# Performance work log

Hardware: AMD Instinct MI355X
Metric: run time of the kernel (lower is better)

Reference implementation:

```python
import jax, jax.numpy as jnp
import numpy as np

DN = ('NCHW', 'OIHW', 'NCHW')

def conv(x, w, b=None, pad=0):
    y = jax.lax.conv_general_dilated(x, w, (1, 1), [(pad, pad), (pad, pad)], dimension_numbers=DN)
    if b is not None:
        y = y + b[None, :, None, None]
    return y

def bn(x, g, b):
    # inference-mode BatchNorm with running_mean=0, running_var=1 (affine only)
    return g[None, :, None, None] * x + b[None, :, None, None]

def gru(msg, h, wg, bg, wc, g, be):
    gates = conv(jnp.concatenate([msg, h], axis=1), wg, bg)  # [B,2,H,W]
    r = jax.nn.sigmoid(gates[:, 0:1])
    u = jax.nn.sigmoid(gates[:, 1:2])
    cnm = jax.nn.leaky_relu(bn(conv(jnp.concatenate([msg, r * h], axis=1), wc), g, be), 0.01)
    return (1.0 - u) * h + u * cnm

def setup_inputs() -> dict:
    key = jax.random.key(0)
    ks = jax.random.split(key, 32)
    B, C, H, W = 8, 10, 192, 192
    s = 0.1
    inp = {
        'f_nodes': jax.random.normal(ks[0], (2, B, C, H, W), jnp.float32),
        'h_nodes': jax.random.normal(ks[1], (3, B, C, H, W), jnp.float32),
        'p_nodes': jax.random.normal(ks[2], (7, B, C, H, W), jnp.float32),
        'xh': jax.random.normal(ks[3], (B, C, H, W), jnp.float32),
        # Decomp_att: 1x1 conv 30->3
        'w_dmap': jax.random.normal(ks[4], (3, 30, 1, 1)) * s,
        'b_dmap': jnp.zeros((3,)),
        # Decomposition relation (shared across 2 children): 3x3 conv 20->10 + BN
        'w_decomp': jax.random.normal(ks[5], (10, 20, 3, 3)) * s,
        'g_decomp': jnp.ones((10,)), 'be_decomp': jnp.zeros((10,)),
        # Comp_att upper: 1x1 conv 40->1 ; lower: 20->1
        'w_cau': jax.random.normal(ks[6], (1, 40, 1, 1)) * s, 'b_cau': jnp.zeros((1,)),
        'w_cal': jax.random.normal(ks[7], (1, 20, 1, 1)) * s, 'b_cal': jnp.zeros((1,)),
        # Composition relation (shared across parts): 3x3 conv 20->10 + BN
        'w_cu': jax.random.normal(ks[8], (10, 20, 3, 3)) * s,
        'g_cu': jnp.ones((10,)), 'be_cu': jnp.zeros((10,)),
        'w_cl': jax.random.normal(ks[9], (10, 20, 3, 3)) * s,
        'g_cl': jnp.ones((10,)), 'be_cl': jnp.zeros((10,)),
        # ConvGRU upper: gates 1x1 20->2, candidate 1x1 20->10 + ABN(leaky_relu)
        'wg_u': jax.random.normal(ks[10], (2, 20, 1, 1)) * s, 'bg_u': jnp.zeros((2,)),
        'wc_u': jax.random.normal(ks[11], (10, 20, 1, 1)) * s,
        'g_u': jnp.ones((10,)), 'be_u': jnp.zeros((10,)),
        # ConvGRU lower
        'wg_l': jax.random.normal(ks[12], (2, 20, 1, 1)) * s, 'bg_l': jnp.zeros((2,)),
        'wc_l': jax.random.normal(ks[13], (10, 20, 1, 1)) * s,
        'g_l': jnp.ones((10,)), 'be_l': jnp.zeros((10,)),
    }
    return inp

def reference(f_nodes, h_nodes, p_nodes, xh,
              w_dmap, b_dmap, w_decomp, g_decomp, be_decomp,
              w_cau, b_cau, w_cal, b_cal,
              w_cu, g_cu, be_cu, w_cl, g_cl, be_cl,
              wg_u, bg_u, wc_u, g_u, be_u,
              wg_l, bg_l, wc_l, g_l, be_l):
    f1 = f_nodes[1]
    h1, h2 = h_nodes[1], h_nodes[2]

    # Decomp_att: 1x1 conv over [f1, h1, h2]
    decomp_map = conv(jnp.concatenate([f1, h1, h2], axis=1), w_dmap, b_dmap)  # [B,3,H,W]
    att = jax.nn.softmax(decomp_map, axis=1)

    # Decomposition (channels 0 is parent-self slot; children use slots 1,2)
    d0 = jax.nn.relu(bn(conv(jnp.concatenate([f1 * att[:, 1:2], h1], axis=1), w_decomp, pad=1), g_decomp, be_decomp))
    d1 = jax.nn.relu(bn(conv(jnp.concatenate([f1 * att[:, 2:3], h2], axis=1), w_decomp, pad=1), g_decomp, be_decomp))

    # Upper half: parts 1..4
    upper = [p_nodes[i] for i in (1, 2, 3, 4)]
    comp_map_u = jax.nn.sigmoid(conv(jnp.concatenate(upper, axis=1), w_cau, b_cau))  # [B,1,H,W]
    comp_u = sum(jax.nn.relu(bn(conv(jnp.concatenate([h1, c * comp_map_u], axis=1), w_cu, pad=1), g_cu, be_cu)) for c in upper)
    msg_u = d0 + comp_u
    xh_u = gru(msg_u, h1, wg_u, bg_u, wc_u, g_u, be_u)

    # Lower half: parts 5..6
    lower = [p_nodes[i] for i in (5, 6)]
    comp_map_l = jax.nn.sigmoid(conv(jnp.concatenate(lower, axis=1), w_cal, b_cal))
    comp_l = sum(jax.nn.relu(bn(conv(jnp.concatenate([h2, c * comp_map_l], axis=1), w_cl, pad=1), g_cl, be_cl)) for c in lower)
    msg_l = d1 + comp_l
    xh_l = gru(msg_l, h2, wg_l, bg_l, wc_l, g_l, be_l)

    xh_new = jnp.stack([h_nodes[0], xh_u, xh_l], axis=0)  # [3,B,10,H,W]
    return (xh_new, decomp_map, comp_map_u, comp_map_l)
```

## Files before the change

kernel.cpp:

```cpp
#include <hip/hip_runtime.h>

#define HW 36864
#define WD 192
#define BB 8
#define CC 10
#define PW 194
#define PB ((size_t)(PW*PW*16))
#define PA ((size_t)BB*PB)

typedef __attribute__((ext_vector_type(8))) short short8;
typedef __attribute__((ext_vector_type(4))) float f32x4;

__device__ __forceinline__ short f2bf(float v) {
    unsigned u = __float_as_uint(v);
    unsigned r = (u + 0x7fffu + ((u >> 16) & 1u)) >> 16;
    return (short)r;
}
__device__ __forceinline__ float b2f(short s) {
    return __uint_as_float(((unsigned)(unsigned short)s) << 16);
}

#define ASYNC16(gp, lp) __builtin_amdgcn_global_load_lds( \
    (const __attribute__((address_space(1))) void*)(gp),  \
    (__attribute__((address_space(3))) void*)(lp), 16, 0, 0)

__device__ __forceinline__ void store16(short* d, const float* v, float s) {
    short8 lo, hi;
    #pragma unroll
    for (int i = 0; i < 8; ++i) lo[i] = f2bf(v[i]*s);
    hi = (short8){f2bf(v[8]*s), f2bf(v[9]*s), 0,0,0,0,0,0};
    *(short8*)d = lo;
    *(short8*)(d+8) = hi;
}

__global__ __launch_bounds__(256) void prep_kernel(
    const float* __restrict__ f_nodes, const float* __restrict__ h_nodes,
    const float* __restrict__ p_nodes,
    const float* __restrict__ w_dmap, const float* __restrict__ b_dmap,
    const float* __restrict__ w_cau, const float* __restrict__ b_cau,
    const float* __restrict__ w_cal, const float* __restrict__ b_cal,
    float* __restrict__ out, short* __restrict__ ws)
{
    int t = blockIdx.x*256 + threadIdx.x;
    if (t >= BB*PW*PW) return;
    int b  = t / (PW*PW);
    int pp = t - b*(PW*PW);
    int py = pp / PW, px = pp - py*PW;
    short* wb = ws + (size_t)b*PB + (size_t)pp*16;

    if (py == 0 || py == PW-1 || px == 0 || px == PW-1) {
        short8 z = (short8){0,0,0,0,0,0,0,0};
        #pragma unroll
        for (int a = 0; a < 10; ++a) {
            *(short8*)(wb + (size_t)a*PA)     = z;
            *(short8*)(wb + (size_t)a*PA + 8) = z;
        }
        return;
    }
    int sp = (py-1)*WD + (px-1);

    const float* f1 = f_nodes + ((size_t)(BB   + b))*CC*HW + sp;
    const float* h0 = h_nodes + ((size_t)(       b))*CC*HW + sp;
    const float* h1 = h_nodes + ((size_t)(BB   + b))*CC*HW + sp;
    const float* h2 = h_nodes + ((size_t)(2*BB + b))*CC*HW + sp;

    float fv[10], av[10], bv[10];
    #pragma unroll
    for (int c = 0; c < 10; ++c) {
        fv[c] = f1[(size_t)c*HW];
        av[c] = h1[(size_t)c*HW];
        bv[c] = h2[(size_t)c*HW];
    }

    const size_t O1 = (size_t)3*BB*CC*HW;
    const size_t O2 = O1 + (size_t)BB*3*HW;
    const size_t O3 = O2 + (size_t)BB*HW;

    float dm[3];
    #pragma unroll
    for (int j = 0; j < 3; ++j) {
        float s = b_dmap[j];
        #pragma unroll
        for (int c = 0; c < 10; ++c) s = fmaf(w_dmap[j*30 + c],      fv[c], s);
        #pragma unroll
        for (int c = 0; c < 10; ++c) s = fmaf(w_dmap[j*30 + 10 + c], av[c], s);
        #pragma unroll
        for (int c = 0; c < 10; ++c) s = fmaf(w_dmap[j*30 + 20 + c], bv[c], s);
        dm[j] = s;
        out[O1 + ((size_t)b*3 + j)*HW + sp] = s;
    }
    float mx = fmaxf(dm[0], fmaxf(dm[1], dm[2]));
    float e0 = expf(dm[0]-mx), e1 = expf(dm[1]-mx), e2 = expf(dm[2]-mx);
    float inv = 1.f / (e0 + e1 + e2);
    float a1 = e1*inv, a2 = e2*inv;

    store16(wb + 0*PA, av, 1.f);
    store16(wb + 1*PA, bv, 1.f);
    store16(wb + 2*PA, fv, a1);
    store16(wb + 3*PA, fv, a2);

    float* o0 = out + (size_t)b*CC*HW + sp;
    #pragma unroll
    for (int c = 0; c < 10; ++c) o0[(size_t)c*HW] = h0[(size_t)c*HW];

    {
        float pv[4][10];
        float su = b_cau[0];
        #pragma unroll
        for (int i = 0; i < 4; ++i) {
            const float* p = p_nodes + ((size_t)((1+i)*BB + b))*CC*HW + sp;
            #pragma unroll
            for (int c = 0; c < 10; ++c) pv[i][c] = p[(size_t)c*HW];
            #pragma unroll
            for (int c = 0; c < 10; ++c) su = fmaf(w_cau[i*10 + c], pv[i][c], su);
        }
        float cmU = 1.f / (1.f + expf(-su));
        out[O2 + (size_t)b*HW + sp] = cmU;
        #pragma unroll
        for (int i = 0; i < 4; ++i) store16(wb + (size_t)(4+i)*PA, pv[i], cmU);
    }
    {
        float qv[2][10];
        float sl = b_cal[0];
        #pragma unroll
        for (int i = 0; i < 2; ++i) {
            const float* p = p_nodes + ((size_t)((5+i)*BB + b))*CC*HW + sp;
            #pragma unroll
            for (int c = 0; c < 10; ++c) qv[i][c] = p[(size_t)c*HW];
            #pragma unroll
            for (int c = 0; c < 10; ++c) sl = fmaf(w_cal[i*10 + c], qv[i][c], sl);
        }
        float cmL = 1.f / (1.f + expf(-sl));
        out[O3 + (size_t)b*HW + sp] = cmL;
        #pragma unroll
        for (int i = 0; i < 2; ++i) store16(wb + (size_t)(8+i)*PA, qv[i], cmL);
    }
}

__device__ __forceinline__ void dma_tile(short* lds, const short* g,
                                         int tid, int y0, int x0)
{
    #pragma unroll
    for (int r = 0; r < 3; ++r) {
        int idx = r*256 + tid;
        int row = idx / 36;
        int col = idx - row*36;
        size_t go = (idx < 648) ? (((size_t)(y0+row)*PW + x0)*16 + (size_t)col*8)
                                : (size_t)0;
        ASYNC16(g + go, lds + (size_t)idx*8);
    }
}

__global__ __launch_bounds__(256) void half_kernel(
    const short* __restrict__ ws,
    const float* __restrict__ w_dec, const float* __restrict__ gD, const float* __restrict__ bD,
    const float* __restrict__ w_cu, const float* __restrict__ gCu, const float* __restrict__ bCu,
    const float* __restrict__ w_cl, const float* __restrict__ gCl, const float* __restrict__ bCl,
    const float* __restrict__ wg_u, const float* __restrict__ bg_u, const float* __restrict__ wc_u,
    const float* __restrict__ g_u, const float* __restrict__ be_u,
    const float* __restrict__ wg_l, const float* __restrict__ bg_l, const float* __restrict__ wc_l,
    const float* __restrict__ g_l, const float* __restrict__ be_l,
    float* __restrict__ out)
{
    __shared__ __align__(16) short sTh[6144];
    __shared__ __align__(16) short sTp0[6144];
    __shared__ __align__(16) short sTp1[6144];
    __shared__ __align__(16) short sWb[4*2688];
    __shared__ float sMsg[256*13];
    __shared__ float sPar[302];

    const int tid  = threadIdx.x;
    const int lane = tid & 63;
    const int w    = tid >> 6;
    const int g    = lane >> 4;
    const int n    = lane & 15;
    const int half = blockIdx.z >> 3;
    const int b    = blockIdx.z & 7;
    const int x0   = blockIdx.x*16, y0 = blockIdx.y*16;

    const float* w_cmp = half ? w_cl : w_cu;
    const float* gC  = half ? gCl  : gCu;
    const float* bC  = half ? bCl  : bCu;
    const float* wg  = half ? wg_l : wg_u;
    const float* bg  = half ? bg_l : bg_u;
    const float* wc  = half ? wc_l : wc_u;
    const float* gG  = half ? g_l  : g_u;
    const float* beG = half ? be_l : be_u;
    const int nparts = half ? 2 : 4;

    const short* hArr  = ws + (size_t)half*PA     + (size_t)b*PB;
    const short* fArr  = ws + (size_t)(2+half)*PA + (size_t)b*PB;
    const short* pArr0 = ws + (size_t)(4+half*4)*PA + (size_t)b*PB;

    for (int i = tid; i < 4*2688/2; i += 256) ((int*)sWb)[i] = 0;
    dma_tile(sTh,  hArr,  tid, y0, x0);
    dma_tile(sTp0, fArr,  tid, y0, x0);
    dma_tile(sTp1, pArr0, tid, y0, x0);
    __syncthreads();

    for (int i = tid; i < 1800; i += 256) {
        int o = i/180, r = i - o*180, ci = r/9, kp = r - ci*9;
        int c  = (ci < 10) ? ci : ci - 10;
        int s2 = (ci < 10) ? 0 : 1;
        sWb[s2*2688     + o*168 + kp*16 + c] = f2bf(w_dec[i]);
        sWb[(2+s2)*2688 + o*168 + kp*16 + c] = f2bf(w_cmp[i]);
    }
    if (tid < 10) {
        sPar[tid]    = gD[tid];  sPar[10+tid] = bD[tid];
        sPar[20+tid] = gC[tid];  sPar[30+tid] = bC[tid];
        sPar[40+tid] = gG[tid];  sPar[50+tid] = beG[tid];
    }
    if (tid < 40) sPar[60+tid]  = wg[tid];
    if (tid < 2)  sPar[100+tid] = bg[tid];
    if (tid >= 56 && tid < 256) sPar[102+(tid-56)] = (tid-56 < 200) ? wc[tid-56] : 0.f;
    __syncthreads();

    int aoff[5];
    #pragma unroll
    for (int t5 = 0; t5 < 5; ++t5) {
        int k  = 32*t5 + 8*g;
        int kp = k >> 4;
        int c8 = k & 15;
        if (kp < 9) { int ky = kp/3, kx = kp - ky*3; aoff[t5] = (ky*18 + kx + n)*16 + c8; }
        else        aoff[t5] = 0;
    }
    const int wbase = w*4*288;

    short8 bF[5], bH[5], bCh[5], bCp[5];
    #pragma unroll
    for (int t5 = 0; t5 < 5; ++t5) {
        int ko = 32*t5 + 8*g;
        bF[t5]  = *(const short8*)(sWb + 0*2688 + n*168 + ko);
        bH[t5]  = *(const short8*)(sWb + 1*2688 + n*168 + ko);
        bCh[t5] = *(const short8*)(sWb + 2*2688 + n*168 + ko);
        bCp[t5] = *(const short8*)(sWb + 3*2688 + n*168 + ko);
    }

    f32x4 accD[4], accH[4];
    #pragma unroll
    for (int mt = 0; mt < 4; ++mt) { accD[mt] = (f32x4){0,0,0,0}; accH[mt] = (f32x4){0,0,0,0}; }
    #pragma unroll
    for (int t5 = 0; t5 < 5; ++t5) {
        #pragma unroll
        for (int mt = 0; mt < 4; ++mt) {
            short8 a = *(const short8*)(sTp0 + wbase + mt*288 + aoff[t5]);
            accD[mt] = __builtin_amdgcn_mfma_f32_16x16x32_bf16(a, bF[t5], accD[mt], 0,0,0);
        }
    }
    #pragma unroll
    for (int t5 = 0; t5 < 5; ++t5) {
        #pragma unroll
        for (int mt = 0; mt < 4; ++mt) {
            short8 a = *(const short8*)(sTh + wbase + mt*288 + aoff[t5]);
            accD[mt] = __builtin_amdgcn_mfma_f32_16x16x32_bf16(a, bH[t5],  accD[mt], 0,0,0);
            accH[mt] = __builtin_amdgcn_mfma_f32_16x16x32_bf16(a, bCh[t5], accH[mt], 0,0,0);
        }
    }
    const int np = (n < 10) ? n : 9;
    const float gDv = sPar[np],    bDv = sPar[10+np];
    const float gCv = sPar[20+np], bCv = sPar[30+np];
    f32x4 msgf[4];
    #pragma unroll
    for (int mt = 0; mt < 4; ++mt)
        #pragma unroll
        for (int j = 0; j < 4; ++j)
            msgf[mt][j] = fmaxf(fmaf(gDv, accD[mt][j], bDv), 0.f);
    __syncthreads();

    for (int j = 0; j < nparts; ++j) {
        if (j+1 < nparts)
            dma_tile((j&1) ? sTp1 : sTp0, pArr0 + (size_t)(j+1)*PA, tid, y0, x0);
        const short* cur = (j&1) ? sTp0 : sTp1;
        f32x4 acc[4];
        #pragma unroll
        for (int mt = 0; mt < 4; ++mt) acc[mt] = (f32x4){0,0,0,0};
        #pragma unroll
        for (int t5 = 0; t5 < 5; ++t5) {
            #pragma unroll
            for (int mt = 0; mt < 4; ++mt) {
                short8 a = *(const short8*)(cur + wbase + mt*288 + aoff[t5]);
                acc[mt] = __builtin_amdgcn_mfma_f32_16x16x32_bf16(a, bCp[t5], acc[mt], 0,0,0);
            }
        }
        #pragma unroll
        for (int mt = 0; mt < 4; ++mt)
            #pragma unroll
            for (int jj = 0; jj < 4; ++jj)
                msgf[mt][jj] += fmaxf(fmaf(gCv, accH[mt][jj] + acc[mt][jj], bCv), 0.f);
        __syncthreads();
    }

    if (n < 10) {
        #pragma unroll
        for (int mt = 0; mt < 4; ++mt)
            #pragma unroll
            for (int r2 = 0; r2 < 4; ++r2)
                sMsg[((4*w + mt)*16 + 4*g + r2)*13 + n] = msgf[mt][r2];
    }
    __syncthreads();

    {
        int row = tid >> 4, xx = tid & 15;
        int gy = y0 + row, gx = x0 + xx;
        float msg[10], hc[10];
        #pragma unroll
        for (int c = 0; c < 10; ++c) msg[c] = sMsg[tid*13 + c];
        #pragma unroll
        for (int c = 0; c < 10; ++c) hc[c] = b2f(sTh[((row+1)*18 + (xx+1))*16 + c]);

        float g0 = sPar[100], g1 = sPar[101];
        #pragma unroll
        for (int c = 0; c < 10; ++c) {
            g0 = fmaf(sPar[60+c], msg[c], g0);
            g1 = fmaf(sPar[80+c], msg[c], g1);
        }
        #pragma unroll
        for (int c = 0; c < 10; ++c) {
            g0 = fmaf(sPar[70+c], hc[c], g0);
            g1 = fmaf(sPar[90+c], hc[c], g1);
        }
        float r = 1.f / (1.f + expf(-g0));
        float u = 1.f / (1.f + expf(-g1));

        float* op = out + (size_t)(1+half)*BB*CC*HW + (size_t)b*CC*HW + gy*WD + gx;
        #pragma unroll
        for (int o = 0; o < 10; ++o) {
            float s = 0.f;
            const float* wr = &sPar[102 + o*20];
            #pragma unroll
            for (int c = 0; c < 10; ++c) s = fmaf(wr[c], msg[c], s);
            #pragma unroll
            for (int c = 0; c < 10; ++c) s = fmaf(wr[10+c], r*hc[c], s);
            s = fmaf(sPar[40+o], s, sPar[50+o]);
            s = (s > 0.f) ? s : 0.01f*s;
            op[(size_t)o*HW] = (1.f - u)*hc[o] + u*s;
        }
    }
}

extern "C" void kernel_launch(void* const* d_in, const int* in_sizes, int n_in,
                              void* d_out, int out_size, void* d_ws, size_t ws_size,
                              hipStream_t stream)
{
    const float* f_nodes = (const float*)d_in[0];
    const float* h_nodes = (const float*)d_in[1];
    const float* p_nodes = (const float*)d_in[2];
    const float* w_dmap   = (const float*)d_in[4];
    const float* b_dmap   = (const float*)d_in[5];
    const float* w_decomp = (const float*)d_in[6];
    const float* g_decomp = (const float*)d_in[7];
    const float* be_decomp= (const float*)d_in[8];
    const float* w_cau    = (const float*)d_in[9];
    const float* b_cau    = (const float*)d_in[10];
    const float* w_cal    = (const float*)d_in[11];
    const float* b_cal    = (const float*)d_in[12];
    const float* w_cu     = (const float*)d_in[13];
    const float* g_cu     = (const float*)d_in[14];
    const float* be_cu    = (const float*)d_in[15];
    const float* w_cl     = (const float*)d_in[16];
    const float* g_cl     = (const float*)d_in[17];
    const float* be_cl    = (const float*)d_in[18];
    const float* wg_u     = (const float*)d_in[19];
    const float* bg_u     = (const float*)d_in[20];
    const float* wc_u     = (const float*)d_in[21];
    const float* g_u      = (const float*)d_in[22];
    const float* be_u     = (const float*)d_in[23];
    const float* wg_l     = (const float*)d_in[24];
    const float* bg_l     = (const float*)d_in[25];
    const float* wc_l     = (const float*)d_in[26];
    const float* g_l      = (const float*)d_in[27];
    const float* be_l     = (const float*)d_in[28];

    float* out = (float*)d_out;
    short* ws  = (short*)d_ws;

    prep_kernel<<<dim3((BB*PW*PW + 255)/256), dim3(256), 0, stream>>>(
        f_nodes, h_nodes, p_nodes, w_dmap, b_dmap,
        w_cau, b_cau, w_cal, b_cal, out, ws);

    half_kernel<<<dim3(WD/16, WD/16, 16), dim3(256), 0, stream>>>(
        ws, w_decomp, g_decomp, be_decomp,
        w_cu, g_cu, be_cu, w_cl, g_cl, be_cl,
        wg_u, bg_u, wc_u, g_u, be_u,
        wg_l, bg_l, wc_l, g_l, be_l,
        out);
}
```

Before: 317.3 us.

## Vectorize prep into float4 work groups and precompute bf16 weights once

The prep kernel now gives each thread four adjacent pixels using float4 loads and stores. Work is split across three block groups (decomposition, upper parts, lower parts), and border zeroing and weight packing go to extra blocks. The conv weights and per-half parameters are converted to bf16 and packed into the workspace once, so half_kernel no longer rebuilds them in LDS in every block. half_kernel reads its B operands straight from global or cache, which removes an LDS buffer and a barrier, at the cost of global reads in the MFMA setup.

```diff
diff --git a/kernel.cpp b/kernel.cpp
--- a/kernel.cpp
+++ b/kernel.cpp
@@ -7,9 +7,13 @@
 #define PW 194
 #define PB ((size_t)(PW*PW*16))
 #define PA ((size_t)BB*PB)
+#define WSW_OFF ((size_t)10*PA)
+#define NWSW 15360
 
 typedef __attribute__((ext_vector_type(8))) short short8;
 typedef __attribute__((ext_vector_type(4))) float f32x4;
+
+__device__ __forceinline__ f32x4 sp4(float x) { return (f32x4){x, x, x, x}; }
 
 __device__ __forceinline__ short f2bf(float v) {
     unsigned u = __float_as_uint(v);
@@ -24,13 +28,17 @@
     (const __attribute__((address_space(1))) void*)(gp),  \
     (__attribute__((address_space(3))) void*)(lp), 16, 0, 0)
 
-__device__ __forceinline__ void store16(short* d, const float* v, float s) {
-    short8 lo, hi;
-    #pragma unroll
-    for (int i = 0; i < 8; ++i) lo[i] = f2bf(v[i]*s);
-    hi = (short8){f2bf(v[8]*s), f2bf(v[9]*s), 0,0,0,0,0,0};
-    *(short8*)d = lo;
-    *(short8*)(d+8) = hi;
+__device__ __forceinline__ void store4(short* d, const f32x4* v, f32x4 s) {
+    #pragma unroll
+    for (int i = 0; i < 4; ++i) {
+        short8 lo = { f2bf(v[0][i]*s[i]), f2bf(v[1][i]*s[i]),
+                      f2bf(v[2][i]*s[i]), f2bf(v[3][i]*s[i]),
+                      f2bf(v[4][i]*s[i]), f2bf(v[5][i]*s[i]),
+                      f2bf(v[6][i]*s[i]), f2bf(v[7][i]*s[i]) };
+        short8 hi = { f2bf(v[8][i]*s[i]), f2bf(v[9][i]*s[i]), 0,0,0,0,0,0 };
+        *(short8*)(d + i*16)     = lo;
+        *(short8*)(d + i*16 + 8) = hi;
+    }
 }
 
 __global__ __launch_bounds__(256) void prep_kernel(
@@ -39,101 +47,172 @@
     const float* __restrict__ w_dmap, const float* __restrict__ b_dmap,
     const float* __restrict__ w_cau, const float* __restrict__ b_cau,
     const float* __restrict__ w_cal, const float* __restrict__ b_cal,
+    const float* __restrict__ w_decomp, const float* __restrict__ w_cu,
+    const float* __restrict__ w_cl,
+    const float* __restrict__ g_decomp, const float* __restrict__ be_decomp,
+    const float* __restrict__ g_cu, const float* __restrict__ be_cu,
+    const float* __restrict__ g_cl, const float* __restrict__ be_cl,
+    const float* __restrict__ wg_u, const float* __restrict__ bg_u,
+    const float* __restrict__ wc_u, const float* __restrict__ g_u,
+    const float* __restrict__ be_u,
+    const float* __restrict__ wg_l, const float* __restrict__ bg_l,
+    const float* __restrict__ wc_l, const float* __restrict__ g_l,
+    const float* __restrict__ be_l,
     float* __restrict__ out, short* __restrict__ ws)
 {
-    int t = blockIdx.x*256 + threadIdx.x;
-    if (t >= BB*PW*PW) return;
-    int b  = t / (PW*PW);
-    int pp = t - b*(PW*PW);
-    int py = pp / PW, px = pp - py*PW;
-    short* wb = ws + (size_t)b*PB + (size_t)pp*16;
-
-    if (py == 0 || py == PW-1 || px == 0 || px == PW-1) {
-        short8 z = (short8){0,0,0,0,0,0,0,0};
-        #pragma unroll
-        for (int a = 0; a < 10; ++a) {
-            *(short8*)(wb + (size_t)a*PA)     = z;
-            *(short8*)(wb + (size_t)a*PA + 8) = z;
-        }
-        return;
-    }
-    int sp = (py-1)*WD + (px-1);
-
-    const float* f1 = f_nodes + ((size_t)(BB   + b))*CC*HW + sp;
-    const float* h0 = h_nodes + ((size_t)(       b))*CC*HW + sp;
-    const float* h1 = h_nodes + ((size_t)(BB   + b))*CC*HW + sp;
-    const float* h2 = h_nodes + ((size_t)(2*BB + b))*CC*HW + sp;
-
-    float fv[10], av[10], bv[10];
-    #pragma unroll
-    for (int c = 0; c < 10; ++c) {
-        fv[c] = f1[(size_t)c*HW];
-        av[c] = h1[(size_t)c*HW];
-        bv[c] = h2[(size_t)c*HW];
-    }
-
+    const int gb  = blockIdx.x;
+    const int tid = threadIdx.x;
     const size_t O1 = (size_t)3*BB*CC*HW;
     const size_t O2 = O1 + (size_t)BB*3*HW;
     const size_t O3 = O2 + (size_t)BB*HW;
 
-    float dm[3];
-    #pragma unroll
-    for (int j = 0; j < 3; ++j) {
-        float s = b_dmap[j];
-        #pragma unroll
-        for (int c = 0; c < 10; ++c) s = fmaf(w_dmap[j*30 + c],      fv[c], s);
-        #pragma unroll
-        for (int c = 0; c < 10; ++c) s = fmaf(w_dmap[j*30 + 10 + c], av[c], s);
-        #pragma unroll
-        for (int c = 0; c < 10; ++c) s = fmaf(w_dmap[j*30 + 20 + c], bv[c], s);
-        dm[j] = s;
-        out[O1 + ((size_t)b*3 + j)*HW + sp] = s;
-    }
-    float mx = fmaxf(dm[0], fmaxf(dm[1], dm[2]));
-    float e0 = expf(dm[0]-mx), e1 = expf(dm[1]-mx), e2 = expf(dm[2]-mx);
-    float inv = 1.f / (e0 + e1 + e2);
-    float a1 = e1*inv, a2 = e2*inv;
-
-    store16(wb + 0*PA, av, 1.f);
-    store16(wb + 1*PA, bv, 1.f);
-    store16(wb + 2*PA, fv, a1);
-    store16(wb + 3*PA, fv, a2);
-
-    float* o0 = out + (size_t)b*CC*HW + sp;
-    #pragma unroll
-    for (int c = 0; c < 10; ++c) o0[(size_t)c*HW] = h0[(size_t)c*HW];
-
-    {
-        float pv[4][10];
-        float su = b_cau[0];
+    if (gb >= 864) {
+        int gi = (gb - 864)*256 + tid;
+        if (gi < 8*772) {
+            int b = gi / 772, r = gi - b*772;
+            int py, px;
+            if      (r < 194) { py = 0;       px = r;       }
+            else if (r < 388) { py = 193;     px = r - 194; }
+            else if (r < 580) { py = r - 387; px = 0;       }
+            else              { py = r - 579; px = 193;     }
+            short* wb = ws + (size_t)b*PB + ((size_t)py*PW + px)*16;
+            short8 z = (short8){0,0,0,0,0,0,0,0};
+            #pragma unroll
+            for (int a = 0; a < 10; ++a) {
+                *(short8*)(wb + (size_t)a*PA)     = z;
+                *(short8*)(wb + (size_t)a*PA + 8) = z;
+            }
+        }
+        if (gb == 864) {
+            short* wsW = ws + WSW_OFF;
+            for (int i = tid; i < NWSW/2; i += 256) ((int*)wsW)[i] = 0;
+            __syncthreads();
+            for (int i = tid; i < 1800; i += 256) {
+                int o = i/180, r = i - o*180, ci = r/9, kp = r - ci*9;
+                int c  = (ci < 10) ? ci : ci - 10;
+                int s2 = (ci < 10) ? 0 : 1;
+                wsW[(size_t)s2*2560     + o*160 + kp*16 + c] = f2bf(w_decomp[i]);
+                wsW[(size_t)(2+s2)*2560 + o*160 + kp*16 + c] = f2bf(w_cu[i]);
+                wsW[(size_t)(4+s2)*2560 + o*160 + kp*16 + c] = f2bf(w_cl[i]);
+            }
+            float* wsP = (float*)(ws + WSW_OFF + NWSW);
+            #pragma unroll
+            for (int hf = 0; hf < 2; ++hf) {
+                float* P = wsP + hf*302;
+                const float* gC  = hf ? g_cl  : g_cu;
+                const float* bC  = hf ? be_cl : be_cu;
+                const float* gG  = hf ? g_l   : g_u;
+                const float* beG = hf ? be_l  : be_u;
+                const float* wg  = hf ? wg_l  : wg_u;
+                const float* bg  = hf ? bg_l  : bg_u;
+                const float* wc  = hf ? wc_l  : wc_u;
+                if (tid < 10) {
+                    P[tid]    = g_decomp[tid];  P[10+tid] = be_decomp[tid];
+                    P[20+tid] = gC[tid];        P[30+tid] = bC[tid];
+                    P[40+tid] = gG[tid];        P[50+tid] = beG[tid];
+                }
+                if (tid < 40) P[60+tid]  = wg[tid];
+                if (tid < 2)  P[100+tid] = bg[tid];
+                for (int i = tid; i < 200; i += 256) P[102+i] = wc[i];
+            }
+        }
+        return;
+    }
+
+    const int grp = gb / 288;
+    const int i0  = (gb - grp*288)*256 + tid;
+    const int xq  = i0 % 48;
+    const int y   = (i0 / 48) % 192;
+    const int b   = i0 / 9216;
+    const int sp  = y*WD + 4*xq;
+    short* wb = ws + (size_t)b*PB + ((size_t)(y+1)*PW + 4*xq + 1)*16;
+
+    if (grp == 0) {
+        const float* f1 = f_nodes + ((size_t)(BB   + b))*CC*HW + sp;
+        const float* h0 = h_nodes + ((size_t)        b )*CC*HW + sp;
+        const float* h1 = h_nodes + ((size_t)(BB   + b))*CC*HW + sp;
+        const float* h2 = h_nodes + ((size_t)(2*BB + b))*CC*HW + sp;
+
+        {
+            #pragma unroll
+            for (int c = 0; c < 10; ++c)
+                *(f32x4*)(out + (size_t)b*CC*HW + (size_t)c*HW + sp) =
+                    *(const f32x4*)(h0 + (size_t)c*HW);
+        }
+        f32x4 fv[10], av[10], bv[10];
+        #pragma unroll
+        for (int c = 0; c < 10; ++c) {
+            fv[c] = *(const f32x4*)(f1 + (size_t)c*HW);
+            av[c] = *(const f32x4*)(h1 + (size_t)c*HW);
+            bv[c] = *(const f32x4*)(h2 + (size_t)c*HW);
+        }
+        f32x4 dm[3];
+        #pragma unroll
+        for (int j = 0; j < 3; ++j) {
+            f32x4 s = sp4(b_dmap[j]);
+            #pragma unroll
+            for (int c = 0; c < 10; ++c) s += sp4(w_dmap[j*30 + c])      * fv[c];
+            #pragma unroll
+            for (int c = 0; c < 10; ++c) s += sp4(w_dmap[j*30 + 10 + c]) * av[c];
+            #pragma unroll
+            for (int c = 0; c < 10; ++c) s += sp4(w_dmap[j*30 + 20 + c]) * bv[c];
+            dm[j] = s;
+            *(f32x4*)(out + O1 + ((size_t)b*3 + j)*HW + sp) = s;
+        }
+        f32x4 a1, a2;
+        #pragma unroll
+        for (int i = 0; i < 4; ++i) {
+            float m  = fmaxf(dm[0][i], fmaxf(dm[1][i], dm[2][i]));
+            float e0 = expf(dm[0][i]-m), e1 = expf(dm[1][i]-m), e2 = expf(dm[2][i]-m);
+            float inv = 1.f / (e0 + e1 + e2);
+            a1[i] = e1*inv; a2[i] = e2*inv;
+        }
+        store4(wb + 0*PA, av, sp4(1.f));
+        store4(wb + 1*PA, bv, sp4(1.f));
+        store4(wb + 2*PA, fv, a1);
+        store4(wb + 3*PA, fv, a2);
+    } else if (grp == 1) {
+        f32x4 su = sp4(b_cau[0]);
         #pragma unroll
         for (int i = 0; i < 4; ++i) {
             const float* p = p_nodes + ((size_t)((1+i)*BB + b))*CC*HW + sp;
             #pragma unroll
-            for (int c = 0; c < 10; ++c) pv[i][c] = p[(size_t)c*HW];
-            #pragma unroll
-            for (int c = 0; c < 10; ++c) su = fmaf(w_cau[i*10 + c], pv[i][c], su);
-        }
-        float cmU = 1.f / (1.f + expf(-su));
-        out[O2 + (size_t)b*HW + sp] = cmU;
-        #pragma unroll
-        for (int i = 0; i < 4; ++i) store16(wb + (size_t)(4+i)*PA, pv[i], cmU);
-    }
-    {
-        float qv[2][10];
-        float sl = b_cal[0];
+            for (int c = 0; c < 10; ++c)
+                su += sp4(w_cau[i*10 + c]) * (*(const f32x4*)(p + (size_t)c*HW));
+        }
+        f32x4 cm;
+        #pragma unroll
+        for (int i = 0; i < 4; ++i) cm[i] = 1.f / (1.f + expf(-su[i]));
+        *(f32x4*)(out + O2 + (size_t)b*HW + sp) = cm;
+        #pragma unroll
+        for (int i = 0; i < 4; ++i) {
+            const float* p = p_nodes + ((size_t)((1+i)*BB + b))*CC*HW + sp;
+            f32x4 pv[10];
+            #pragma unroll
+            for (int c = 0; c < 10; ++c) pv[c] = *(const f32x4*)(p + (size_t)c*HW);
+            store4(wb + (size_t)(4+i)*PA, pv, cm);
+        }
+    } else {
+        f32x4 sl = sp4(b_cal[0]);
         #pragma unroll
         for (int i = 0; i < 2; ++i) {
             const float* p = p_nodes + ((size_t)((5+i)*BB + b))*CC*HW + sp;
             #pragma unroll
-            for (int c = 0; c < 10; ++c) qv[i][c] = p[(size_t)c*HW];
-            #pragma unroll
-            for (int c = 0; c < 10; ++c) sl = fmaf(w_cal[i*10 + c], qv[i][c], sl);
-        }
-        float cmL = 1.f / (1.f + expf(-sl));
-        out[O3 + (size_t)b*HW + sp] = cmL;
-        #pragma unroll
-        for (int i = 0; i < 2; ++i) store16(wb + (size_t)(8+i)*PA, qv[i], cmL);
+            for (int c = 0; c < 10; ++c)
+                sl += sp4(w_cal[i*10 + c]) * (*(const f32x4*)(p + (size_t)c*HW));
+        }
+        f32x4 cm;
+        #pragma unroll
+        for (int i = 0; i < 4; ++i) cm[i] = 1.f / (1.f + expf(-sl[i]));
+        *(f32x4*)(out + O3 + (size_t)b*HW + sp) = cm;
+        #pragma unroll
+        for (int i = 0; i < 2; ++i) {
+            const float* p = p_nodes + ((size_t)((5+i)*BB + b))*CC*HW + sp;
+            f32x4 pv[10];
+            #pragma unroll
+            for (int c = 0; c < 10; ++c) pv[c] = *(const f32x4*)(p + (size_t)c*HW);
+            store4(wb + (size_t)(8+i)*PA, pv, cm);
+        }
     }
 }
 
@@ -152,20 +231,11 @@
 }
 
 __global__ __launch_bounds__(256) void half_kernel(
-    const short* __restrict__ ws,
-    const float* __restrict__ w_dec, const float* __restrict__ gD, const float* __restrict__ bD,
-    const float* __restrict__ w_cu, const float* __restrict__ gCu, const float* __restrict__ bCu,
-    const float* __restrict__ w_cl, const float* __restrict__ gCl, const float* __restrict__ bCl,
-    const float* __restrict__ wg_u, const float* __restrict__ bg_u, const float* __restrict__ wc_u,
-    const float* __restrict__ g_u, const float* __restrict__ be_u,
-    const float* __restrict__ wg_l, const float* __restrict__ bg_l, const float* __restrict__ wc_l,
-    const float* __restrict__ g_l, const float* __restrict__ be_l,
-    float* __restrict__ out)
+    const short* __restrict__ ws, float* __restrict__ out)
 {
     __shared__ __align__(16) short sTh[6144];
     __shared__ __align__(16) short sTp0[6144];
     __shared__ __align__(16) short sTp1[6144];
-    __shared__ __align__(16) short sWb[4*2688];
     __shared__ float sMsg[256*13];
     __shared__ float sPar[302];
 
@@ -177,84 +247,61 @@
     const int half = blockIdx.z >> 3;
     const int b    = blockIdx.z & 7;
     const int x0   = blockIdx.x*16, y0 = blockIdx.y*16;
-
-    const float* w_cmp = half ? w_cl : w_cu;
-    const float* gC  = half ? gCl  : gCu;
-    const float* bC  = half ? bCl  : bCu;
-    const float* wg  = half ? wg_l : wg_u;
-    const float* bg  = half ? bg_l : bg_u;
-    const float* wc  = half ? wc_l : wc_u;
-    const float* gG  = half ? g_l  : g_u;
-    const float* beG = half ? be_l : be_u;
     const int nparts = half ? 2 : 4;
 
-    const short* hArr  = ws + (size_t)half*PA     + (size_t)b*PB;
-    const short* fArr  = ws + (size_t)(2+half)*PA + (size_t)b*PB;
-    const short* pArr0 = ws + (size_t)(4+half*4)*PA + (size_t)b*PB;
-
-    for (int i = tid; i < 4*2688/2; i += 256) ((int*)sWb)[i] = 0;
+    const short* hArr  = ws + (size_t)half*PA       + (size_t)b*PB;
+    const short* fArr  = ws + (size_t)(2+half)*PA   + (size_t)b*PB;
+    const short* pArr0 = ws + (size_t)(4+4*half)*PA + (size_t)b*PB;
+    const short* wsW   = ws + WSW_OFF;
+    const float* wsP   = (const float*)(ws + WSW_OFF + NWSW) + half*302;
+
     dma_tile(sTh,  hArr,  tid, y0, x0);
     dma_tile(sTp0, fArr,  tid, y0, x0);
     dma_tile(sTp1, pArr0, tid, y0, x0);
-    __syncthreads();
-
-    for (int i = tid; i < 1800; i += 256) {
-        int o = i/180, r = i - o*180, ci = r/9, kp = r - ci*9;
-        int c  = (ci < 10) ? ci : ci - 10;
-        int s2 = (ci < 10) ? 0 : 1;
-        sWb[s2*2688     + o*168 + kp*16 + c] = f2bf(w_dec[i]);
-        sWb[(2+s2)*2688 + o*168 + kp*16 + c] = f2bf(w_cmp[i]);
-    }
-    if (tid < 10) {
-        sPar[tid]    = gD[tid];  sPar[10+tid] = bD[tid];
-        sPar[20+tid] = gC[tid];  sPar[30+tid] = bC[tid];
-        sPar[40+tid] = gG[tid];  sPar[50+tid] = beG[tid];
-    }
-    if (tid < 40) sPar[60+tid]  = wg[tid];
-    if (tid < 2)  sPar[100+tid] = bg[tid];
-    if (tid >= 56 && tid < 256) sPar[102+(tid-56)] = (tid-56 < 200) ? wc[tid-56] : 0.f;
-    __syncthreads();
+
+    for (int i = tid; i < 302; i += 256) sPar[i] = wsP[i];
 
     int aoff[5];
     #pragma unroll
     for (int t5 = 0; t5 < 5; ++t5) {
         int k  = 32*t5 + 8*g;
-        int kp = k >> 4;
-        int c8 = k & 15;
+        int kp = k >> 4, c8 = k & 15;
         if (kp < 9) { int ky = kp/3, kx = kp - ky*3; aoff[t5] = (ky*18 + kx + n)*16 + c8; }
         else        aoff[t5] = 0;
     }
     const int wbase = w*4*288;
 
-    short8 bF[5], bH[5], bCh[5], bCp[5];
-    #pragma unroll
-    for (int t5 = 0; t5 < 5; ++t5) {
-        int ko = 32*t5 + 8*g;
-        bF[t5]  = *(const short8*)(sWb + 0*2688 + n*168 + ko);
-        bH[t5]  = *(const short8*)(sWb + 1*2688 + n*168 + ko);
-        bCh[t5] = *(const short8*)(sWb + 2*2688 + n*168 + ko);
-        bCp[t5] = *(const short8*)(sWb + 3*2688 + n*168 + ko);
-    }
+    __syncthreads();
 
     f32x4 accD[4], accH[4];
     #pragma unroll
-    for (int mt = 0; mt < 4; ++mt) { accD[mt] = (f32x4){0,0,0,0}; accH[mt] = (f32x4){0,0,0,0}; }
-    #pragma unroll
-    for (int t5 = 0; t5 < 5; ++t5) {
-        #pragma unroll
-        for (int mt = 0; mt < 4; ++mt) {
-            short8 a = *(const short8*)(sTp0 + wbase + mt*288 + aoff[t5]);
-            accD[mt] = __builtin_amdgcn_mfma_f32_16x16x32_bf16(a, bF[t5], accD[mt], 0,0,0);
-        }
-    }
-    #pragma unroll
-    for (int t5 = 0; t5 < 5; ++t5) {
-        #pragma unroll
-        for (int mt = 0; mt < 4; ++mt) {
-            short8 a = *(const short8*)(sTh + wbase + mt*288 + aoff[t5]);
-            accD[mt] = __builtin_amdgcn_mfma_f32_16x16x32_bf16(a, bH[t5],  accD[mt], 0,0,0);
-            accH[mt] = __builtin_amdgcn_mfma_f32_16x16x32_bf16(a, bCh[t5], accH[mt], 0,0,0);
-        }
+    for (int mt = 0; mt < 4; ++mt) {
+        accD[mt] = (f32x4){0.f,0.f,0.f,0.f};
+        accH[mt] = (f32x4){0.f,0.f,0.f,0.f};
+    }
+    {
+        short8 bF[5], bH[5], bCh[5];
+        #pragma unroll
+        for (int t5 = 0; t5 < 5; ++t5) {
+            bF[t5]  = *(const short8*)(wsW + (size_t)0*2560 + n*160 + 32*t5 + 8*g);
+            bH[t5]  = *(const short8*)(wsW + (size_t)1*2560 + n*160 + 32*t5 + 8*g);
+            bCh[t5] = *(const short8*)(wsW + (size_t)(2+2*half)*2560 + n*160 + 32*t5 + 8*g);
+        }
+        #pragma unroll
+        for (int t5 = 0; t5 < 5; ++t5)
+            #pragma unroll
+            for (int mt = 0; mt < 4; ++mt) {
+                short8 a = *(const short8*)(sTp0 + wbase + mt*288 + aoff[t5]);
+                accD[mt] = __builtin_amdgcn_mfma_f32_16x16x32_bf16(a, bF[t5], accD[mt], 0,0,0);
+            }
+        #pragma unroll
+        for (int t5 = 0; t5 < 5; ++t5)
+            #pragma unroll
+            for (int mt = 0; mt < 4; ++mt) {
+                short8 a = *(const short8*)(sTh + wbase + mt*288 + aoff[t5]);
+                accD[mt] = __builtin_amdgcn_mfma_f32_16x16x32_bf16(a, bH[t5],  accD[mt], 0,0,0);
+                accH[mt] = __builtin_amdgcn_mfma_f32_16x16x32_bf16(a, bCh[t5], accH[mt], 0,0,0);
+            }
     }
     const int np = (n < 10) ? n : 9;
     const float gDv = sPar[np],    bDv = sPar[10+np];
@@ -266,6 +313,11 @@
         for (int j = 0; j < 4; ++j)
             msgf[mt][j] = fmaxf(fmaf(gDv, accD[mt][j], bDv), 0.f);
     __syncthreads();
+
+    short8 bCp[5];
+    #pragma unroll
+    for (int t5 = 0; t5 < 5; ++t5)
+        bCp[t5] = *(const short8*)(wsW + (size_t)(3+2*half)*2560 + n*160 + 32*t5 + 8*g);
 
     for (int j = 0; j < nparts; ++j) {
         if (j+1 < nparts)
@@ -273,15 +325,14 @@
         const short* cur = (j&1) ? sTp0 : sTp1;
         f32x4 acc[4];
         #pragma unroll
-        for (int mt = 0; mt < 4; ++mt) acc[mt] = (f32x4){0,0,0,0};
-        #pragma unroll
-        for (int t5 = 0; t5 < 5; ++t5) {
+        for (int mt = 0; mt < 4; ++mt) acc[mt] = (f32x4){0.f,0.f,0.f,0.f};
+        #pragma unroll
+        for (int t5 = 0; t5 < 5; ++t5)
             #pragma unroll
             for (int mt = 0; mt < 4; ++mt) {
                 short8 a = *(const short8*)(cur + wbase + mt*288 + aoff[t5]);
                 acc[mt] = __builtin_amdgcn_mfma_f32_16x16x32_bf16(a, bCp[t5], acc[mt], 0,0,0);
             }
-        }
         #pragma unroll
         for (int mt = 0; mt < 4; ++mt)
             #pragma unroll
@@ -374,14 +425,14 @@
     float* out = (float*)d_out;
     short* ws  = (short*)d_ws;
 
-    prep_kernel<<<dim3((BB*PW*PW + 255)/256), dim3(256), 0, stream>>>(
+    prep_kernel<<<dim3(896), dim3(256), 0, stream>>>(
         f_nodes, h_nodes, p_nodes, w_dmap, b_dmap,
-        w_cau, b_cau, w_cal, b_cal, out, ws);
-
-    half_kernel<<<dim3(WD/16, WD/16, 16), dim3(256), 0, stream>>>(
-        ws, w_decomp, g_decomp, be_decomp,
-        w_cu, g_cu, be_cu, w_cl, g_cl, be_cl,
+        w_cau, b_cau, w_cal, b_cal,
+        w_decomp, w_cu, w_cl,
+        g_decomp, be_decomp, g_cu, be_cu, g_cl, be_cl,
         wg_u, bg_u, wc_u, g_u, be_u,
         wg_l, bg_l, wc_l, g_l, be_l,
-        out);
-}
+        out, ws);
+
+    half_kernel<<<dim3(WD/16, WD/16, 16), dim3(256), 0, stream>>>(ws, out);
+}
```

New measurement: 318.6 us. No clear change (+0.4%).
